# Kernel tuning notes

Hardware: AMD Instinct MI355X
Metric: run time of the kernel (lower is better)

The kernel has to match this reference:

```python
import jax, jax.numpy as jnp
import numpy as np

EMBED_DIM = 2048
NUM_HEADS = 16
HEAD_DIM = EMBED_DIM // NUM_HEADS
CACHE_LEN = 8192


def setup_inputs() -> dict:
    key = jax.random.key(0)
    ks = jax.random.split(key, 11)
    s = 1.0 / np.sqrt(EMBED_DIM)
    return {
        "x": jax.random.normal(ks[0], (EMBED_DIM,), jnp.float32),
        "v": jax.random.normal(ks[1], (CACHE_LEN, NUM_HEADS, HEAD_DIM), jnp.float32),
        "k": jax.random.normal(ks[2], (CACHE_LEN, NUM_HEADS, HEAD_DIM), jnp.float32),
        "Wv": jax.random.normal(ks[3], (EMBED_DIM, EMBED_DIM), jnp.float32) * s,
        "bv": jnp.zeros((EMBED_DIM,), jnp.float32),
        "Wq": jax.random.normal(ks[4], (EMBED_DIM, EMBED_DIM), jnp.float32) * s,
        "bq": jnp.zeros((EMBED_DIM,), jnp.float32),
        "Wk": jax.random.normal(ks[5], (EMBED_DIM, EMBED_DIM), jnp.float32) * s,
        "bk": jnp.zeros((EMBED_DIM,), jnp.float32),
        "Wo": jax.random.normal(ks[6], (EMBED_DIM, EMBED_DIM), jnp.float32) * s,
        "bo": jnp.zeros((EMBED_DIM,), jnp.float32),
    }


def reference(x, v, k, Wv, bv, Wq, bq, Wk, bk, Wo, bo):
    H, Dh = NUM_HEADS, HEAD_DIM
    # project the single token into q/k/v, new k/v appended to the cache
    v_i = (x @ Wv + bv).reshape(1, H, Dh)
    q_i = (x @ Wq + bq).reshape(H, Dh)
    k_i = (x @ Wk + bk).reshape(1, H, Dh)
    v = jnp.concatenate((v, v_i), axis=0)  # [L+1, H, Dh]
    k = jnp.concatenate((k, k_i), axis=0)  # [L+1, H, Dh]
    # single-query attention over the full cache
    attn = jnp.einsum('hd,khd->hk', q_i, k) / jnp.sqrt(jnp.asarray(Dh, x.dtype))
    attn = jax.nn.softmax(attn, axis=-1)
    values = jnp.einsum('hk,khd->hd', attn, v).reshape(H * Dh)
    out_i = values @ Wo + bo
    return (out_i, v, k)
```

## Files before the change

### kernel.cpp

```cpp
#include <hip/hip_runtime.h>
#include <math.h>

#define E   2048
#define H   16
#define DH  128
#define L   8192
#define L1  8193
#define SS  8256

#define WS_Q    0
#define WS_KI   2048
#define WS_VI   4096
#define WS_ACC  6144
#define WS_SC   8192
#define WS_M    (WS_SC + H * SS)
#define WS_SUM  (WS_M + 16)

__global__ __launch_bounds__(256) void init_kernel(const float* __restrict__ bq,
                                                   const float* __restrict__ bk,
                                                   const float* __restrict__ bv,
                                                   const float* __restrict__ bo,
                                                   float* __restrict__ ws,
                                                   float* __restrict__ out) {
    int j = blockIdx.x * 256 + threadIdx.x;
    if (j < E) {
        ws[WS_Q  + j] = bq[j];
        ws[WS_KI + j] = bk[j];
        ws[WS_VI + j] = bv[j];
        ws[WS_ACC + j] = 0.f;
        out[j] = bo[j];
    }
}

__global__ __launch_bounds__(256) void proj_kernel(const float* __restrict__ x,
                                                   const float* __restrict__ Wq,
                                                   const float* __restrict__ Wk,
                                                   const float* __restrict__ Wv,
                                                   float* __restrict__ ws) {
    const int JB = E / 256;
    const int KC = E / 128;
    int b = blockIdx.x;
    int m = b / (JB * KC);
    int r = b % (JB * KC);
    int jb = r / KC, kc = r % KC;
    const float* W = (m == 0) ? Wq : (m == 1) ? Wk : Wv;
    float* dst = ws + ((m == 0) ? WS_Q : (m == 1) ? WS_KI : WS_VI);

    __shared__ float xs[128];
    int t = threadIdx.x;
    if (t < 128) xs[t] = x[kc * 128 + t];
    __syncthreads();

    int j = jb * 256 + t;
    const float* Wp = W + (size_t)(kc * 128) * E + j;
    float acc = 0.f;
#pragma unroll 8
    for (int i = 0; i < 128; ++i) acc += xs[i] * Wp[(size_t)i * E];
    atomicAdd(dst + j, acc);
}

__global__ __launch_bounds__(256) void score_kernel(const float* __restrict__ kcache,
                                                    float* __restrict__ ws,
                                                    float* __restrict__ out_k) {
    int wave = threadIdx.x >> 6;
    int lane = threadIdx.x & 63;
    int p = blockIdx.x * 4 + wave;
    if (p >= H * L1) return;
    int l = p >> 4;
    int h = p & 15;

    float2 kv;
    if (l < L) kv = *(const float2*)(kcache + ((size_t)l * H + h) * DH + lane * 2);
    else       kv = *(const float2*)(ws + WS_KI + h * DH + lane * 2);
    *(float2*)(out_k + ((size_t)l * H + h) * DH + lane * 2) = kv;

    float2 qv = *(const float2*)(ws + WS_Q + h * DH + lane * 2);
    float d = qv.x * kv.x + qv.y * kv.y;
#pragma unroll
    for (int off = 32; off > 0; off >>= 1) d += __shfl_down(d, off);
    if (lane == 0) ws[WS_SC + h * SS + l] = d * 0.08838834764831845f;
}

__global__ __launch_bounds__(256) void smax_kernel(float* __restrict__ ws) {
    int h = blockIdx.x;
    int t = threadIdx.x;
    __shared__ float red[256];
    const float* s = ws + WS_SC + h * SS;

    float m = -INFINITY;
    for (int l = t; l < L1; l += 256) m = fmaxf(m, s[l]);
    red[t] = m; __syncthreads();
    for (int o = 128; o > 0; o >>= 1) {
        if (t < o) red[t] = fmaxf(red[t], red[t + o]);
        __syncthreads();
    }
    m = red[0]; __syncthreads();

    float sum = 0.f;
    for (int l = t; l < L1; l += 256) sum += __expf(s[l] - m);
    red[t] = sum; __syncthreads();
    for (int o = 128; o > 0; o >>= 1) {
        if (t < o) red[t] += red[t + o];
        __syncthreads();
    }
    if (t == 0) { ws[WS_M + h] = m; ws[WS_SUM + h] = 1.f / red[0]; }
}

__global__ __launch_bounds__(256) void pv_kernel(const float* __restrict__ vcache,
                                                 float* __restrict__ ws,
                                                 float* __restrict__ out_v) {
    int h = blockIdx.y;
    int c = blockIdx.x;
    int t = threadIdx.x;
    int d = t & 127;
    int half = t >> 7;
    int l0 = c * 128;
    int lend = min(l0 + 128, L1);
    float m   = ws[WS_M + h];
    float inv = ws[WS_SUM + h];

    float acc = 0.f;
    for (int l = l0 + half; l < lend; l += 2) {
        float w = __expf(ws[WS_SC + h * SS + l] - m) * inv;
        float vv;
        if (l < L) vv = vcache[((size_t)l * H + h) * DH + d];
        else       vv = ws[WS_VI + h * DH + d];
        out_v[((size_t)l * H + h) * DH + d] = vv;
        acc += w * vv;
    }
    __shared__ float red[256];
    red[t] = acc; __syncthreads();
    if (t < 128) atomicAdd(ws + WS_ACC + h * DH + d, red[t] + red[t + 128]);
}

__global__ __launch_bounds__(256) void outproj_kernel(const float* __restrict__ Wo,
                                                      const float* __restrict__ ws,
                                                      float* __restrict__ out) {
    const int KC = E / 128;
    int jb = blockIdx.x / KC, kc = blockIdx.x % KC;
    __shared__ float xs[128];
    int t = threadIdx.x;
    if (t < 128) xs[t] = ws[WS_ACC + kc * 128 + t];
    __syncthreads();

    int j = jb * 256 + t;
    const float* Wp = Wo + (size_t)(kc * 128) * E + j;
    float a = 0.f;
#pragma unroll 8
    for (int i = 0; i < 128; ++i) a += xs[i] * Wp[(size_t)i * E];
    atomicAdd(out + j, a);
}

extern "C" void kernel_launch(void* const* d_in, const int* in_sizes, int n_in,
                              void* d_out, int out_size, void* d_ws, size_t ws_size,
                              hipStream_t stream) {
    const float* x  = (const float*)d_in[0];
    const float* v  = (const float*)d_in[1];
    const float* k  = (const float*)d_in[2];
    const float* Wv = (const float*)d_in[3];
    const float* bv = (const float*)d_in[4];
    const float* Wq = (const float*)d_in[5];
    const float* bq = (const float*)d_in[6];
    const float* Wk = (const float*)d_in[7];
    const float* bk = (const float*)d_in[8];
    const float* Wo = (const float*)d_in[9];
    const float* bo = (const float*)d_in[10];
    float* out = (float*)d_out;
    float* ws  = (float*)d_ws;
    float* out_v = out + E;
    float* out_k = out + E + (size_t)L1 * E;

    init_kernel<<<8, 256, 0, stream>>>(bq, bk, bv, bo, ws, out);
    proj_kernel<<<3 * 8 * 16, 256, 0, stream>>>(x, Wq, Wk, Wv, ws);
    score_kernel<<<(H * L1 + 3) / 4, 256, 0, stream>>>(k, ws, out_k);
    smax_kernel<<<16, 256, 0, stream>>>(ws);
    pv_kernel<<<dim3((L1 + 127) / 128, H), 256, 0, stream>>>(v, ws, out_v);
    outproj_kernel<<<8 * 16, 256, 0, stream>>>(Wo, ws, out);
}
```

Measured before the change: 341.4 us.

## Fuse score, softmax and PV into split-K flash-decode attention kernel

Replaces the separate score, softmax and PV kernels with one attention kernel. Each block handles 64 keys of one head, computes local max, sum and weighted V partials, and a finalize kernel merges the partials. The projection and output-projection kernels switch to float4 loads with a different tile shape. This removes the score round trip through workspace and two launches, and widens memory accesses. It adds a partials buffer and a small serial merge over 129 chunks per head.

```diff
diff --git a/kernel.cpp b/kernel.cpp
--- a/kernel.cpp
+++ b/kernel.cpp
@@ -6,15 +6,14 @@
 #define DH  128
 #define L   8192
 #define L1  8193
-#define SS  8256
-
-#define WS_Q    0
-#define WS_KI   2048
-#define WS_VI   4096
-#define WS_ACC  6144
-#define WS_SC   8192
-#define WS_M    (WS_SC + H * SS)
-#define WS_SUM  (WS_M + 16)
+#define NC  129
+#define PSTR 132
+
+#define WS_Q      0
+#define WS_KI     2048
+#define WS_VI     4096
+#define WS_VAL    6144
+#define WS_PART   8192
 
 __global__ __launch_bounds__(256) void init_kernel(const float* __restrict__ bq,
                                                    const float* __restrict__ bk,
@@ -27,7 +26,6 @@
         ws[WS_Q  + j] = bq[j];
         ws[WS_KI + j] = bk[j];
         ws[WS_VI + j] = bv[j];
-        ws[WS_ACC + j] = 0.f;
         out[j] = bo[j];
     }
 }
@@ -37,118 +35,150 @@
                                                    const float* __restrict__ Wk,
                                                    const float* __restrict__ Wv,
                                                    float* __restrict__ ws) {
-    const int JB = E / 256;
-    const int KC = E / 128;
     int b = blockIdx.x;
-    int m = b / (JB * KC);
-    int r = b % (JB * KC);
-    int jb = r / KC, kc = r % KC;
+    int m = b >> 6;
+    int r = b & 63;
+    int jb = r >> 5, kc = r & 31;
     const float* W = (m == 0) ? Wq : (m == 1) ? Wk : Wv;
     float* dst = ws + ((m == 0) ? WS_Q : (m == 1) ? WS_KI : WS_VI);
 
-    __shared__ float xs[128];
+    __shared__ float xs[64];
     int t = threadIdx.x;
-    if (t < 128) xs[t] = x[kc * 128 + t];
-    __syncthreads();
-
-    int j = jb * 256 + t;
-    const float* Wp = W + (size_t)(kc * 128) * E + j;
-    float acc = 0.f;
+    if (t < 64) xs[t] = x[kc * 64 + t];
+    __syncthreads();
+
+    int j = jb * 1024 + t * 4;
+    const float* Wp = W + (size_t)(kc * 64) * E + j;
+    float4 a = make_float4(0.f, 0.f, 0.f, 0.f);
 #pragma unroll 8
-    for (int i = 0; i < 128; ++i) acc += xs[i] * Wp[(size_t)i * E];
-    atomicAdd(dst + j, acc);
-}
-
-__global__ __launch_bounds__(256) void score_kernel(const float* __restrict__ kcache,
-                                                    float* __restrict__ ws,
-                                                    float* __restrict__ out_k) {
-    int wave = threadIdx.x >> 6;
-    int lane = threadIdx.x & 63;
-    int p = blockIdx.x * 4 + wave;
-    if (p >= H * L1) return;
-    int l = p >> 4;
-    int h = p & 15;
-
-    float2 kv;
-    if (l < L) kv = *(const float2*)(kcache + ((size_t)l * H + h) * DH + lane * 2);
-    else       kv = *(const float2*)(ws + WS_KI + h * DH + lane * 2);
-    *(float2*)(out_k + ((size_t)l * H + h) * DH + lane * 2) = kv;
-
-    float2 qv = *(const float2*)(ws + WS_Q + h * DH + lane * 2);
-    float d = qv.x * kv.x + qv.y * kv.y;
-#pragma unroll
-    for (int off = 32; off > 0; off >>= 1) d += __shfl_down(d, off);
-    if (lane == 0) ws[WS_SC + h * SS + l] = d * 0.08838834764831845f;
-}
-
-__global__ __launch_bounds__(256) void smax_kernel(float* __restrict__ ws) {
-    int h = blockIdx.x;
-    int t = threadIdx.x;
-    __shared__ float red[256];
-    const float* s = ws + WS_SC + h * SS;
-
-    float m = -INFINITY;
-    for (int l = t; l < L1; l += 256) m = fmaxf(m, s[l]);
-    red[t] = m; __syncthreads();
-    for (int o = 128; o > 0; o >>= 1) {
-        if (t < o) red[t] = fmaxf(red[t], red[t + o]);
-        __syncthreads();
-    }
-    m = red[0]; __syncthreads();
-
-    float sum = 0.f;
-    for (int l = t; l < L1; l += 256) sum += __expf(s[l] - m);
-    red[t] = sum; __syncthreads();
-    for (int o = 128; o > 0; o >>= 1) {
-        if (t < o) red[t] += red[t + o];
-        __syncthreads();
-    }
-    if (t == 0) { ws[WS_M + h] = m; ws[WS_SUM + h] = 1.f / red[0]; }
-}
-
-__global__ __launch_bounds__(256) void pv_kernel(const float* __restrict__ vcache,
-                                                 float* __restrict__ ws,
-                                                 float* __restrict__ out_v) {
+    for (int i = 0; i < 64; ++i) {
+        float4 w4 = *(const float4*)(Wp + (size_t)i * E);
+        float xi = xs[i];
+        a.x += xi * w4.x; a.y += xi * w4.y; a.z += xi * w4.z; a.w += xi * w4.w;
+    }
+    atomicAdd(dst + j,     a.x);
+    atomicAdd(dst + j + 1, a.y);
+    atomicAdd(dst + j + 2, a.z);
+    atomicAdd(dst + j + 3, a.w);
+}
+
+__global__ __launch_bounds__(256) void attn_kernel(const float* __restrict__ kcache,
+                                                   const float* __restrict__ vcache,
+                                                   float* __restrict__ ws,
+                                                   float* __restrict__ out_k,
+                                                   float* __restrict__ out_v) {
     int h = blockIdx.y;
     int c = blockIdx.x;
     int t = threadIdx.x;
-    int d = t & 127;
-    int half = t >> 7;
-    int l0 = c * 128;
-    int lend = min(l0 + 128, L1);
-    float m   = ws[WS_M + h];
-    float inv = ws[WS_SUM + h];
-
-    float acc = 0.f;
-    for (int l = l0 + half; l < lend; l += 2) {
-        float w = __expf(ws[WS_SC + h * SS + l] - m) * inv;
-        float vv;
-        if (l < L) vv = vcache[((size_t)l * H + h) * DH + d];
-        else       vv = ws[WS_VI + h * DH + d];
-        out_v[((size_t)l * H + h) * DH + d] = vv;
-        acc += w * vv;
-    }
-    __shared__ float red[256];
-    red[t] = acc; __syncthreads();
-    if (t < 128) atomicAdd(ws + WS_ACC + h * DH + d, red[t] + red[t + 128]);
+    int lane = t & 31;
+    int slot = t >> 5;
+    int d4 = lane * 4;
+
+    __shared__ float sc_lds[64];
+    __shared__ float sred[8];
+    __shared__ float4 racc[256];
+
+    float4 qv = *(const float4*)(ws + WS_Q + h * DH + d4);
+
+    float sc[8];
+    int base = c * 64;
+#pragma unroll
+    for (int i = 0; i < 8; ++i) {
+        int key = base + i * 8 + slot;
+        bool valid = key < L1;
+        float4 kv = make_float4(0.f, 0.f, 0.f, 0.f);
+        if (valid) {
+            const float* src = (key < L) ? (kcache + ((size_t)key * H + h) * DH + d4)
+                                         : (ws + WS_KI + h * DH + d4);
+            kv = *(const float4*)src;
+            *(float4*)(out_k + ((size_t)key * H + h) * DH + d4) = kv;
+        }
+        float d = qv.x * kv.x + qv.y * kv.y + qv.z * kv.z + qv.w * kv.w;
+        d += __shfl_xor(d, 16); d += __shfl_xor(d, 8);
+        d += __shfl_xor(d, 4);  d += __shfl_xor(d, 2); d += __shfl_xor(d, 1);
+        sc[i] = valid ? d * 0.08838834764831845f : -INFINITY;
+        if (lane == 0) sc_lds[i * 8 + slot] = sc[i];
+    }
+    __syncthreads();
+
+    float m = -INFINITY;
+#pragma unroll
+    for (int j = 0; j < 64; ++j) m = fmaxf(m, sc_lds[j]);
+    float ps = 0.f;
+#pragma unroll
+    for (int i = 0; i < 8; ++i) ps += __expf(sc[i] - m);
+    if (lane == 0) sred[slot] = ps;
+    __syncthreads();
+    float s = 0.f;
+#pragma unroll
+    for (int j = 0; j < 8; ++j) s += sred[j];
+
+    float4 acc = make_float4(0.f, 0.f, 0.f, 0.f);
+#pragma unroll
+    for (int i = 0; i < 8; ++i) {
+        int key = base + i * 8 + slot;
+        if (key < L1) {
+            const float* src = (key < L) ? (vcache + ((size_t)key * H + h) * DH + d4)
+                                         : (ws + WS_VI + h * DH + d4);
+            float4 vv = *(const float4*)src;
+            *(float4*)(out_v + ((size_t)key * H + h) * DH + d4) = vv;
+            float w = __expf(sc[i] - m);
+            acc.x += w * vv.x; acc.y += w * vv.y; acc.z += w * vv.z; acc.w += w * vv.w;
+        }
+    }
+    racc[t] = acc;
+    __syncthreads();
+#pragma unroll
+    for (int o = 128; o >= 32; o >>= 1) {
+        if (t < o) {
+            float4 b = racc[t + o];
+            racc[t].x += b.x; racc[t].y += b.y; racc[t].z += b.z; racc[t].w += b.w;
+        }
+        __syncthreads();
+    }
+    float* part = ws + WS_PART + ((size_t)h * NC + c) * PSTR;
+    if (t < 32) *(float4*)(part + t * 4) = racc[t];
+    if (t == 0) { part[128] = m; part[129] = s; }
+}
+
+__global__ __launch_bounds__(128) void finalize_kernel(float* __restrict__ ws) {
+    int h = blockIdx.x;
+    int d = threadIdx.x;
+    const float* ph = ws + WS_PART + (size_t)h * NC * PSTR;
+    float M = -INFINITY;
+    for (int c = 0; c < NC; ++c) M = fmaxf(M, ph[c * PSTR + 128]);
+    float S = 0.f, val = 0.f;
+    for (int c = 0; c < NC; ++c) {
+        float e = __expf(ph[c * PSTR + 128] - M);
+        S   += ph[c * PSTR + 129] * e;
+        val += ph[c * PSTR + d] * e;
+    }
+    ws[WS_VAL + h * DH + d] = val / S;
 }
 
 __global__ __launch_bounds__(256) void outproj_kernel(const float* __restrict__ Wo,
                                                       const float* __restrict__ ws,
                                                       float* __restrict__ out) {
-    const int KC = E / 128;
-    int jb = blockIdx.x / KC, kc = blockIdx.x % KC;
-    __shared__ float xs[128];
+    int b = blockIdx.x;
+    int jb = b >> 5, kc = b & 31;
+    __shared__ float xs[64];
     int t = threadIdx.x;
-    if (t < 128) xs[t] = ws[WS_ACC + kc * 128 + t];
-    __syncthreads();
-
-    int j = jb * 256 + t;
-    const float* Wp = Wo + (size_t)(kc * 128) * E + j;
-    float a = 0.f;
+    if (t < 64) xs[t] = ws[WS_VAL + kc * 64 + t];
+    __syncthreads();
+
+    int j = jb * 1024 + t * 4;
+    const float* Wp = Wo + (size_t)(kc * 64) * E + j;
+    float4 a = make_float4(0.f, 0.f, 0.f, 0.f);
 #pragma unroll 8
-    for (int i = 0; i < 128; ++i) a += xs[i] * Wp[(size_t)i * E];
-    atomicAdd(out + j, a);
+    for (int i = 0; i < 64; ++i) {
+        float4 w4 = *(const float4*)(Wp + (size_t)i * E);
+        float xi = xs[i];
+        a.x += xi * w4.x; a.y += xi * w4.y; a.z += xi * w4.z; a.w += xi * w4.w;
+    }
+    atomicAdd(out + j,     a.x);
+    atomicAdd(out + j + 1, a.y);
+    atomicAdd(out + j + 2, a.z);
+    atomicAdd(out + j + 3, a.w);
 }
 
 extern "C" void kernel_launch(void* const* d_in, const int* in_sizes, int n_in,
@@ -171,9 +201,8 @@
     float* out_k = out + E + (size_t)L1 * E;
 
     init_kernel<<<8, 256, 0, stream>>>(bq, bk, bv, bo, ws, out);
-    proj_kernel<<<3 * 8 * 16, 256, 0, stream>>>(x, Wq, Wk, Wv, ws);
-    score_kernel<<<(H * L1 + 3) / 4, 256, 0, stream>>>(k, ws, out_k);
-    smax_kernel<<<16, 256, 0, stream>>>(ws);
-    pv_kernel<<<dim3((L1 + 127) / 128, H), 256, 0, stream>>>(v, ws, out_v);
-    outproj_kernel<<<8 * 16, 256, 0, stream>>>(Wo, ws, out);
-}
+    proj_kernel<<<192, 256, 0, stream>>>(x, Wq, Wk, Wv, ws);
+    attn_kernel<<<dim3(NC, H), 256, 0, stream>>>(k, v, ws, out_k, out_v);
+    finalize_kernel<<<16, 128, 0, stream>>>(ws);
+    outproj_kernel<<<64, 256, 0, stream>>>(Wo, ws, out);
+}
```

Result: slower. 348.5 us (+2.1%).
